# Optimization experiments

Measured on AMD Instinct MI355X. Metric: run time of the kernel, lower is better.

Reference implementation:

```python
import jax, jax.numpy as jnp
import numpy as np

B, T, D = 2, 4096, 512
H = 8
HD = D // H


def setup_inputs() -> dict:
    key = jax.random.key(0)
    ks = jax.random.split(key, 6)
    s = 0.02
    return {
        "token_embed": jax.random.normal(ks[0], (B, T, D), jnp.float32),
        "Wq": jax.random.normal(ks[1], (D, D), jnp.float32) * s,
        "Wk": jax.random.normal(ks[2], (D, D), jnp.float32) * s,
        "Wv": jax.random.normal(ks[3], (D, D), jnp.float32) * s,
        "Wo": jax.random.normal(ks[4], (D, D), jnp.float32) * s,
        "bo": jnp.zeros((D,), jnp.float32),
    }


def reference(token_embed, Wq, Wk, Wv, Wo, bo):
    b, t, d_in = token_embed.shape
    # QKV projections (Linear without bias): x @ W^T with W stored [d_out, d_in]
    q = jnp.einsum("btd,ed->bte", token_embed, Wq).reshape(b, t, H, HD).transpose(0, 2, 1, 3)
    k = jnp.einsum("btd,ed->bte", token_embed, Wk).reshape(b, t, H, HD).transpose(0, 2, 1, 3)
    v = jnp.einsum("btd,ed->bte", token_embed, Wv).reshape(b, t, H, HD).transpose(0, 2, 1, 3)
    # Scores [b, h, t, t] with causal mask applied before scaling (as in source)
    scores = jnp.einsum("bhqd,bhkd->bhqk", q, k)
    causal = jnp.tril(jnp.ones((t, t), bool))  # True = keep
    scores = jnp.where(causal, scores, -jnp.inf)
    attn = jax.nn.softmax(scores / jnp.sqrt(jnp.float32(HD)), axis=-1)
    # dropout p=0.0 -> identity
    ctx = jnp.einsum("bhqk,bhkd->bhqd", attn, v)
    ctx = ctx.transpose(0, 2, 1, 3).reshape(b, t, H * HD)
    return jnp.einsum("btd,ed->bte", ctx, Wo) + bo
```

## Files before the change

### kernel.cpp

```cpp
#include <hip/hip_runtime.h>

#define B_  2
#define T_  4096
#define D_  512
#define H_  8
#define HD_ 64
#define M_  (B_*T_)

typedef _Float16 h16;
typedef _Float16 v8h __attribute__((ext_vector_type(8)));
typedef _Float16 v4h __attribute__((ext_vector_type(4)));
typedef _Float16 h2  __attribute__((ext_vector_type(2)));
typedef float v4f __attribute__((ext_vector_type(4)));
typedef unsigned short us;
typedef unsigned short us8 __attribute__((ext_vector_type(8)));

union PaU { v8h v; h2 p[4]; };

#define AS1 __attribute__((address_space(1)))
#define AS3 __attribute__((address_space(3)))

__device__ __forceinline__ float bf2f(us u){
  union { unsigned int i; float f; } v; v.i = ((unsigned int)u) << 16; return v.f;
}
__device__ __forceinline__ us f2bf(float f){
  union { float f; unsigned int u; } v; v.f = f;
  unsigned int r = v.u + 0x7FFFu + ((v.u >> 16) & 1u);
  return (us)(r >> 16);
}
__device__ __forceinline__ v4f zero4(){ v4f z; z[0]=0.f; z[1]=0.f; z[2]=0.f; z[3]=0.f; return z; }

__device__ __forceinline__ void glds16(const h16* g, h16* l){
  __builtin_amdgcn_global_load_lds((const AS1 int*)(const void*)g,
                                   (AS3 int*)(void*)l, 16, 0, 0);
}

__device__ __forceinline__ h2 pkrtz(float a, float b){
  auto t = __builtin_amdgcn_cvt_pkrtz(a, b);
  h2 r; __builtin_memcpy(&r, &t, sizeof(r)); return r;
}

#define MFMA32 __builtin_amdgcn_mfma_f32_16x16x32_f16

__global__ __launch_bounds__(256) void conv_all(
    const void* __restrict__ x, const void* __restrict__ w0, const void* __restrict__ w1,
    const void* __restrict__ w2, const void* __restrict__ w3, const void* __restrict__ bo,
    h16* __restrict__ xb, h16* __restrict__ d0, h16* __restrict__ d1,
    h16* __restrict__ d2, h16* __restrict__ d3, float* __restrict__ bof)
{
  const int bid = blockIdx.x, tid = threadIdx.x;
  const void* src; int e0; int seg;
  h16* dst = nullptr;
  if (bid < 2048)      { src = x; e0 = bid * 2048; dst = xb; seg = 0; }
  else if (bid < 2560) {
    const int wsel = (bid - 2048) >> 7;
    src = (wsel == 0) ? w0 : (wsel == 1) ? w1 : (wsel == 2) ? w2 : w3;
    dst = (wsel == 0) ? d0 : (wsel == 1) ? d1 : (wsel == 2) ? d2 : d3;
    e0 = ((bid - 2048) & 127) * 2048; seg = 0;
  } else                { src = bo; e0 = 0; seg = 1; }

  __shared__ int sflag;
  if (tid == 0) sflag = 0;
  __syncthreads();
  const float probe = bf2f(((const us*)src)[e0 + tid]);
  if (!(fabsf(probe) < 1e4f)) atomicAdd(&sflag, 1);
  __syncthreads();
  const int isf32 = (sflag != 0);

  if (seg) {
    if (tid < 64) {
      const int i = tid * 8;
#pragma unroll
      for (int e = 0; e < 8; e++)
        bof[i + e] = isf32 ? ((const float*)src)[i + e] : bf2f(((const us*)src)[i + e]);
    }
    return;
  }
  const int i = e0 + tid * 8;
  float v[8];
  if (isf32) {
    const float* pf = (const float*)src + i;
    const float4 a = *(const float4*)pf;
    const float4 c = *(const float4*)(pf + 4);
    v[0]=a.x; v[1]=a.y; v[2]=a.z; v[3]=a.w; v[4]=c.x; v[5]=c.y; v[6]=c.z; v[7]=c.w;
  } else {
    const us8 u = *(const us8*)((const us*)src + i);
#pragma unroll
    for (int e = 0; e < 8; e++) v[e] = bf2f(u[e]);
  }
  v8h o;
#pragma unroll
  for (int e = 0; e < 8; e++) o[e] = (h16)v[e];
  *(v8h*)(dst + i) = o;
}

__device__ __forceinline__ void stage4(const h16* __restrict__ A, const h16* __restrict__ W,
                                       int m0, int n0, int kk, h16* sA, h16* sB, int tid){
  const int colA = (tid & 3) << 3;
  const int rowT = tid >> 2;
#pragma unroll
  for (int rd = 0; rd < 2; rd++) {
    const int row = rd * 64 + rowT;
    const int f = rd * 2048 + tid * 8;
    glds16(A + (size_t)(m0 + row) * D_ + kk + colA, sA + f);
    glds16(W + (size_t)(n0 + row) * D_ + kk + colA, sB + f);
  }
}

__device__ __forceinline__ void gemm_core(const h16* __restrict__ A,
                                          const h16* __restrict__ W,
                                          int m0, int n0, h16* sA, h16* sB,
                                          v4f acc[4][4]) {
  const int tid = threadIdx.x;
  const int lane = tid & 63, wid = tid >> 6;
  const int r = lane & 15, q = lane >> 4;
#pragma unroll
  for (int i = 0; i < 4; i++)
#pragma unroll
    for (int j = 0; j < 4; j++) acc[i][j] = zero4();

  stage4(A, W, m0, n0, 0, sA, sB, tid);
#pragma unroll 1
  for (int kt = 0; kt < 16; kt++) {
    asm volatile("s_waitcnt vmcnt(0)" ::: "memory");
    asm volatile("s_barrier" ::: "memory");
    if (kt < 15) {
      const int nb = (kt + 1) & 1;
      stage4(A, W, m0, n0, (kt + 1) * 32, sA + nb * 4096, sB + nb * 4096, tid);
    }
    const h16* pA = sA + (kt & 1) * 4096 + ((wid & 1) * 64 + r) * 32 + q * 8;
    const h16* pB = sB + (kt & 1) * 4096 + ((wid >> 1) * 64 + r) * 32 + q * 8;
    v8h a[4], b[4];
#pragma unroll
    for (int i = 0; i < 4; i++) a[i] = *(const v8h*)(pA + i * 512);
#pragma unroll
    for (int j = 0; j < 4; j++) b[j] = *(const v8h*)(pB + j * 512);
    __builtin_amdgcn_s_setprio(1);
#pragma unroll
    for (int i = 0; i < 4; i++)
#pragma unroll
      for (int j = 0; j < 4; j++)
        acc[i][j] = MFMA32(a[i], b[j], acc[i][j], 0, 0, 0);
    __builtin_amdgcn_s_setprio(0);
  }
}

__global__ __launch_bounds__(256, 3) void gemm_qkv(
    const h16* __restrict__ X,
    const h16* __restrict__ Wq, const h16* __restrict__ Wk, const h16* __restrict__ Wv,
    h16* __restrict__ Qo, h16* __restrict__ Ko, h16* __restrict__ VTo)
{
  __shared__ h16 sA[2 * 4096], sB[2 * 4096];
  const h16* W = (blockIdx.z == 0) ? Wq : (blockIdx.z == 1 ? Wk : Wv);
  const int m0 = blockIdx.x * 128, n0 = blockIdx.y * 128;
  v4f acc[4][4];
  gemm_core(X, W, m0, n0, sA, sB, acc);
  const int lane = threadIdx.x & 63, wid = threadIdx.x >> 6;
  const int r = lane & 15, q = lane >> 4;
  const int wm = m0 + (wid & 1) * 64, wn = n0 + (wid >> 1) * 64;
  if (blockIdx.z == 2) {
#pragma unroll
    for (int i = 0; i < 4; i++) {
      const int row0 = wm + i * 16 + q * 4;
      const int bb = row0 >> 12, tt0 = row0 & (T_ - 1);
      const int tpermb = (tt0 & ~63) | (q << 3) | ((i & 1) << 2) | ((i >> 1) << 5);
#pragma unroll
      for (int j = 0; j < 4; j++) {
        const int col = wn + j * 16 + r;
        const int hh = col >> 6, hd = col & 63;
        v4h st;
#pragma unroll
        for (int rr = 0; rr < 4; rr++) st[rr] = (h16)acc[i][j][rr];
        *(v4h*)(VTo + ((size_t)(((bb << 3) + hh) << 6) + hd) * T_ + tpermb) = st;
      }
    }
  } else {
    h16* Y = (blockIdx.z == 0) ? Qo : Ko;
    const float sc = (blockIdx.z == 0) ? 0.1803368801f : 1.0f;
#pragma unroll
    for (int i = 0; i < 4; i++)
#pragma unroll
      for (int j = 0; j < 4; j++)
#pragma unroll
        for (int rr = 0; rr < 4; rr++)
          Y[(size_t)(wm + i*16 + q*4 + rr) * D_ + wn + j*16 + r] = (h16)(acc[i][j][rr] * sc);
  }
}

__global__ __launch_bounds__(256, 3) void gemm_out(
    const h16* __restrict__ A, const h16* __restrict__ W,
    const float* __restrict__ bias, void* __restrict__ out, const void* __restrict__ xprobe)
{
  __shared__ h16 sA[2 * 4096], sB[2 * 4096];
  __shared__ int sflag;
  if (threadIdx.x == 0) sflag = 0;
  __syncthreads();
  const float probe = bf2f(((const us*)xprobe)[threadIdx.x]);
  if (!(fabsf(probe) < 1e4f)) atomicAdd(&sflag, 1);
  __syncthreads();
  const int flag = (sflag != 0);

  const int m0 = blockIdx.x * 128, n0 = blockIdx.y * 128;
  v4f acc[4][4];
  gemm_core(A, W, m0, n0, sA, sB, acc);
  const int lane = threadIdx.x & 63, wid = threadIdx.x >> 6;
  const int r = lane & 15, q = lane >> 4;
  const int wm = m0 + (wid & 1) * 64, wn = n0 + (wid >> 1) * 64;
#pragma unroll
  for (int i = 0; i < 4; i++)
#pragma unroll
    for (int j = 0; j < 4; j++)
#pragma unroll
      for (int rr = 0; rr < 4; rr++) {
        const int row = wm + i*16 + q*4 + rr;
        const int col = wn + j*16 + r;
        const float v = acc[i][j][rr] + bias[col];
        if (flag) ((float*)out)[(size_t)row * D_ + col] = v;
        else ((us*)out)[(size_t)row * D_ + col] = f2bf(v);
      }
}

__global__ __launch_bounds__(256, 4) void attn_kernel(
    const h16* __restrict__ Q, const h16* __restrict__ K,
    const h16* __restrict__ VT, h16* __restrict__ Ctx)
{
  const int h = blockIdx.x;
  const int pos = blockIdx.y + (blockIdx.z << 6);
  const int qc = 63 - (pos >> 1);
  const int b  = pos & 1;
  const int tid = threadIdx.x;
  const int wid = tid >> 6, lane = tid & 63;
  const int r = lane & 15, quad = lane >> 4;
  const int kw = wid & 1, qw = wid >> 1;

  const size_t headoff = (size_t)b * T_ * D_ + (size_t)h * HD_;
  const h16* Qh  = Q + headoff;
  const h16* Kh  = K + headoff;
  const h16* VTh = VT + (size_t)(b * H_ + h) * HD_ * T_;
  h16* Ch = Ctx + headoff;

  __shared__ h16 smem[4][4096];

  const int q0 = qc * 64 + qw * 32;
  const int ntiles = qc + 1;

  const v8h aq00 = *(const v8h*)(Qh + (size_t)(q0 + r) * D_ + quad * 8);
  const v8h aq01 = *(const v8h*)(Qh + (size_t)(q0 + r) * D_ + 32 + quad * 8);
  const v8h aq10 = *(const v8h*)(Qh + (size_t)(q0 + 16 + r) * D_ + quad * 8);
  const v8h aq11 = *(const v8h*)(Qh + (size_t)(q0 + 16 + r) * D_ + 32 + quad * 8);

  v8h vone;
#pragma unroll
  for (int e = 0; e < 8; e++) vone[e] = (h16)1;

  v4f o0[4], o1[4];
#pragma unroll
  for (int j = 0; j < 4; j++) { o0[j] = zero4(); o1[j] = zero4(); }
  v4f ld0 = zero4(), ld1 = zero4();

  const int srow = tid >> 3;
  const int sj = (tid & 7) ^ (srow & 7);
  const h16* kcur = Kh + (size_t)srow * D_ + sj * 8;
  const h16* vcur = VTh + (size_t)srow * T_ + sj * 8;

  glds16(kcur, &smem[0][tid * 8]); glds16(kcur + 32 * D_, &smem[0][2048 + tid * 8]);
  glds16(vcur, &smem[2][tid * 8]); glds16(vcur + 32 * T_, &smem[2][2048 + tid * 8]);
  kcur += 64 * D_; vcur += 64;

  const int xo0 = (quad ^ (r & 7)) * 8;
  const int xo1 = ((quad + 4) ^ (r & 7)) * 8;
  const int xov = ((quad + kw * 4) ^ (r & 7)) * 8;
  const int krow = kw * 32 + r;
  const int kloc = kw * 32 + quad * 4;
  const int qlim0 = qw * 32 + r, qlim1 = qw * 32 + 16 + r;

#define ATT_TILE(CB, MASKED) do {                                              \
    const h16* sKc = smem[(CB)];                                               \
    const h16* sVc = smem[2 + (CB)];                                           \
    const h16* bK = sKc + krow * 64;                                           \
    const v8h ka0 = *(const v8h*)(bK + xo0);                                   \
    const v8h ka1 = *(const v8h*)(bK + xo1);                                   \
    const v8h ka2 = *(const v8h*)(bK + 16 * 64 + xo0);                         \
    const v8h ka3 = *(const v8h*)(bK + 16 * 64 + xo1);                         \
    v8h va[4];                                                                 \
    _Pragma("unroll")                                                          \
    for (int j = 0; j < 4; j++)                                                \
      va[j] = *(const v8h*)(sVc + (j * 16 + r) * 64 + xov);                    \
    v4f s00 = zero4(), s10 = zero4(), s01 = zero4(), s11 = zero4();            \
    __builtin_amdgcn_s_setprio(1);                                             \
    s00 = MFMA32(ka0, aq00, s00, 0,0,0); s00 = MFMA32(ka1, aq01, s00, 0,0,0);  \
    s10 = MFMA32(ka2, aq00, s10, 0,0,0); s10 = MFMA32(ka3, aq01, s10, 0,0,0);  \
    s01 = MFMA32(ka0, aq10, s01, 0,0,0); s01 = MFMA32(ka1, aq11, s01, 0,0,0);  \
    s11 = MFMA32(ka2, aq10, s11, 0,0,0); s11 = MFMA32(ka3, aq11, s11, 0,0,0);  \
    __builtin_amdgcn_s_setprio(0);                                             \
    PaU pa0, pa1;                                                              \
    _Pragma("unroll")                                                          \
    for (int qb = 0; qb < 2; qb++) {                                           \
      const v4f& sa = qb ? s01 : s00;                                          \
      const v4f& sb = qb ? s11 : s10;                                          \
      const int qlim = qb ? qlim1 : qlim0;                                     \
      float e0[4], e1[4];                                                      \
      _Pragma("unroll")                                                        \
      for (int rr = 0; rr < 4; rr++) {                                         \
        float v0 = sa[rr], v1 = sb[rr];                                        \
        if (MASKED) {                                                          \
          if (kloc + rr > qlim)      v0 = -1e30f;                              \
          if (kloc + 16 + rr > qlim) v1 = -1e30f;                              \
        }                                                                      \
        e0[rr] = exp2f(v0); e1[rr] = exp2f(v1);                                \
      }                                                                        \
      PaU* pa = qb ? &pa1 : &pa0;                                              \
      pa->p[0] = pkrtz(e0[0], e0[1]); pa->p[1] = pkrtz(e0[2], e0[3]);          \
      pa->p[2] = pkrtz(e1[0], e1[1]); pa->p[3] = pkrtz(e1[2], e1[3]);          \
    }                                                                          \
    __builtin_amdgcn_s_setprio(1);                                             \
    ld0 = MFMA32(pa0.v, vone, ld0, 0,0,0);                                     \
    ld1 = MFMA32(pa1.v, vone, ld1, 0,0,0);                                     \
    _Pragma("unroll")                                                          \
    for (int j = 0; j < 4; j++) {                                              \
      o0[j] = MFMA32(pa0.v, va[j], o0[j], 0,0,0);                              \
      o1[j] = MFMA32(pa1.v, va[j], o1[j], 0,0,0);                              \
    }                                                                          \
    __builtin_amdgcn_s_setprio(0);                                             \
  } while(0)

#pragma unroll 1
  for (int kt = 0; kt < ntiles - 1; kt++) {
    asm volatile("s_waitcnt vmcnt(0)" ::: "memory");
    asm volatile("s_barrier" ::: "memory");
    const int nb = (kt + 1) & 1;
    glds16(kcur, &smem[nb][tid * 8]);
    glds16(kcur + 32 * D_, &smem[nb][2048 + tid * 8]);
    glds16(vcur, &smem[2 + nb][tid * 8]);
    glds16(vcur + 32 * T_, &smem[2 + nb][2048 + tid * 8]);
    kcur += 64 * D_; vcur += 64;
    ATT_TILE(kt & 1, false);
  }
  asm volatile("s_waitcnt vmcnt(0)" ::: "memory");
  asm volatile("s_barrier" ::: "memory");
  ATT_TILE((ntiles - 1) & 1, true);
#undef ATT_TILE

  __syncthreads();
  float* const red = (float*)&smem[0][0];
  float* const seg = red + qw * 2112;
  float* const lred = red + 4224;
  if (kw) {
#pragma unroll
    for (int hdb = 0; hdb < 4; hdb++)
#pragma unroll
      for (int j = 0; j < 4; j++) {
        seg[(quad * 4 + j) * 66 + hdb * 16 + r] = o0[hdb][j];
        seg[(16 + quad * 4 + j) * 66 + hdb * 16 + r] = o1[hdb][j];
      }
    if (r == 0) {
#pragma unroll
      for (int j = 0; j < 4; j++) {
        lred[qw * 32 + quad * 4 + j] = ld0[j];
        lred[qw * 32 + 16 + quad * 4 + j] = ld1[j];
      }
    }
  }
  __syncthreads();
  if (!kw) {
    float inv0[4], inv1[4];
#pragma unroll
    for (int j = 0; j < 4; j++) {
      inv0[j] = 1.0f / (ld0[j] + lred[qw * 32 + quad * 4 + j]);
      inv1[j] = 1.0f / (ld1[j] + lred[qw * 32 + 16 + quad * 4 + j]);
    }
#pragma unroll
    for (int hdb = 0; hdb < 4; hdb++)
#pragma unroll
      for (int j = 0; j < 4; j++) {
        const float a0 = o0[hdb][j] + seg[(quad * 4 + j) * 66 + hdb * 16 + r];
        const float a1 = o1[hdb][j] + seg[(16 + quad * 4 + j) * 66 + hdb * 16 + r];
        Ch[(size_t)(q0 + quad * 4 + j) * D_ + hdb * 16 + r] = (h16)(a0 * inv0[j]);
        Ch[(size_t)(q0 + 16 + quad * 4 + j) * D_ + hdb * 16 + r] = (h16)(a1 * inv1[j]);
      }
  }
}

extern "C" void kernel_launch(void* const* d_in, const int* in_sizes, int n_in,
                              void* d_out, int out_size, void* d_ws, size_t ws_size,
                              hipStream_t stream) {
  char* ws = (char*)d_ws;
  h16* xb  = (h16*)(ws + 0);
  h16* qb  = (h16*)(ws + 8388608);
  h16* kb  = (h16*)(ws + 16777216);
  h16* vt  = (h16*)(ws + 25165824);
  h16* ctx = (h16*)(ws + 33554432);
  h16* wqb = (h16*)(ws + 41943040);
  h16* wkb = (h16*)(ws + 41943040 + 524288);
  h16* wvb = (h16*)(ws + 41943040 + 2 * 524288);
  h16* wob = (h16*)(ws + 41943040 + 3 * 524288);
  float* bof = (float*)(ws + 41943040 + 4 * 524288);

  conv_all<<<2561, 256, 0, stream>>>(d_in[0], d_in[1], d_in[2], d_in[3], d_in[4],
                                     d_in[5], xb, wqb, wkb, wvb, wob, bof);
  gemm_qkv<<<dim3(M_ / 128, D_ / 128, 3), 256, 0, stream>>>(xb, wqb, wkb, wvb, qb, kb, vt);
  attn_kernel<<<dim3(H_, 64, B_), 256, 0, stream>>>(qb, kb, vt, ctx);
  gemm_out<<<dim3(M_ / 128, D_ / 128, 1), 256, 0, stream>>>(ctx, wob, bof, d_out, d_in[0]);
}
```

Baseline: 172.7 us.

## Shrink GEMM M-tile to 64 and overlap next-tile loads with compute

Both projection GEMMs move from 128x128 to 64x128 block tiles, doubling the grid and raising the occupancy target from 3 to 4 blocks per CU. The staging loop now issues the next k-slice prefetch before waiting, uses a partial vmcnt wait so global loads overlap the MFMA work, and adds a trailing barrier to guard the double buffer. The aim is better CU fill and latency hiding for these small GEMMs, at the cost of lower per-block reuse of the weight tile and an extra barrier per iteration.

```diff
diff --git a/kernel.cpp b/kernel.cpp
--- a/kernel.cpp
+++ b/kernel.cpp
@@ -94,76 +94,76 @@
   *(v8h*)(dst + i) = o;
 }
 
-__device__ __forceinline__ void stage4(const h16* __restrict__ A, const h16* __restrict__ W,
+__device__ __forceinline__ void stage3(const h16* __restrict__ A, const h16* __restrict__ W,
                                        int m0, int n0, int kk, h16* sA, h16* sB, int tid){
-  const int colA = (tid & 3) << 3;
-  const int rowT = tid >> 2;
-#pragma unroll
-  for (int rd = 0; rd < 2; rd++) {
-    const int row = rd * 64 + rowT;
-    const int f = rd * 2048 + tid * 8;
-    glds16(A + (size_t)(m0 + row) * D_ + kk + colA, sA + f);
-    glds16(W + (size_t)(n0 + row) * D_ + kk + colA, sB + f);
-  }
-}
-
-__device__ __forceinline__ void gemm_core(const h16* __restrict__ A,
-                                          const h16* __restrict__ W,
-                                          int m0, int n0, h16* sA, h16* sB,
-                                          v4f acc[4][4]) {
+  const int col = (tid & 3) << 3;
+  const int row = tid >> 2;
+  glds16(A + (size_t)(m0 + row) * D_ + kk + col, sA + tid * 8);
+  glds16(W + (size_t)(n0 + row) * D_ + kk + col, sB + tid * 8);
+  glds16(W + (size_t)(n0 + 64 + row) * D_ + kk + col, sB + 2048 + tid * 8);
+}
+
+__device__ __forceinline__ void gemm_core64(const h16* __restrict__ A,
+                                            const h16* __restrict__ W,
+                                            int m0, int n0, h16* sA, h16* sB,
+                                            v4f acc[2][4]) {
   const int tid = threadIdx.x;
   const int lane = tid & 63, wid = tid >> 6;
   const int r = lane & 15, q = lane >> 4;
 #pragma unroll
-  for (int i = 0; i < 4; i++)
+  for (int i = 0; i < 2; i++)
 #pragma unroll
     for (int j = 0; j < 4; j++) acc[i][j] = zero4();
 
-  stage4(A, W, m0, n0, 0, sA, sB, tid);
+  stage3(A, W, m0, n0, 0, sA, sB, tid);
 #pragma unroll 1
   for (int kt = 0; kt < 16; kt++) {
-    asm volatile("s_waitcnt vmcnt(0)" ::: "memory");
-    asm volatile("s_barrier" ::: "memory");
     if (kt < 15) {
       const int nb = (kt + 1) & 1;
-      stage4(A, W, m0, n0, (kt + 1) * 32, sA + nb * 4096, sB + nb * 4096, tid);
+      stage3(A, W, m0, n0, (kt + 1) * 32, sA + nb * 2048, sB + nb * 4096, tid);
+      asm volatile("s_waitcnt vmcnt(3)" ::: "memory");
+    } else {
+      asm volatile("s_waitcnt vmcnt(0)" ::: "memory");
     }
-    const h16* pA = sA + (kt & 1) * 4096 + ((wid & 1) * 64 + r) * 32 + q * 8;
+    asm volatile("s_barrier" ::: "memory");
+    const h16* pA = sA + (kt & 1) * 2048 + ((wid & 1) * 32 + r) * 32 + q * 8;
     const h16* pB = sB + (kt & 1) * 4096 + ((wid >> 1) * 64 + r) * 32 + q * 8;
-    v8h a[4], b[4];
-#pragma unroll
-    for (int i = 0; i < 4; i++) a[i] = *(const v8h*)(pA + i * 512);
+    v8h a[2], b[4];
+#pragma unroll
+    for (int i = 0; i < 2; i++) a[i] = *(const v8h*)(pA + i * 512);
 #pragma unroll
     for (int j = 0; j < 4; j++) b[j] = *(const v8h*)(pB + j * 512);
     __builtin_amdgcn_s_setprio(1);
 #pragma unroll
-    for (int i = 0; i < 4; i++)
+    for (int i = 0; i < 2; i++)
 #pragma unroll
       for (int j = 0; j < 4; j++)
         acc[i][j] = MFMA32(a[i], b[j], acc[i][j], 0, 0, 0);
     __builtin_amdgcn_s_setprio(0);
-  }
-}
-
-__global__ __launch_bounds__(256, 3) void gemm_qkv(
+    asm volatile("s_barrier" ::: "memory");
+  }
+}
+
+__global__ __launch_bounds__(256, 4) void gemm_qkv(
     const h16* __restrict__ X,
     const h16* __restrict__ Wq, const h16* __restrict__ Wk, const h16* __restrict__ Wv,
     h16* __restrict__ Qo, h16* __restrict__ Ko, h16* __restrict__ VTo)
 {
-  __shared__ h16 sA[2 * 4096], sB[2 * 4096];
+  __shared__ h16 sA[2 * 2048], sB[2 * 4096];
   const h16* W = (blockIdx.z == 0) ? Wq : (blockIdx.z == 1 ? Wk : Wv);
-  const int m0 = blockIdx.x * 128, n0 = blockIdx.y * 128;
-  v4f acc[4][4];
-  gemm_core(X, W, m0, n0, sA, sB, acc);
+  const int m0 = blockIdx.x * 64, n0 = blockIdx.y * 128;
+  v4f acc[2][4];
+  gemm_core64(X, W, m0, n0, sA, sB, acc);
   const int lane = threadIdx.x & 63, wid = threadIdx.x >> 6;
   const int r = lane & 15, q = lane >> 4;
-  const int wm = m0 + (wid & 1) * 64, wn = n0 + (wid >> 1) * 64;
+  const int wm = m0 + (wid & 1) * 32, wn = n0 + (wid >> 1) * 64;
   if (blockIdx.z == 2) {
 #pragma unroll
-    for (int i = 0; i < 4; i++) {
+    for (int i = 0; i < 2; i++) {
+      const int iold = (wid & 1) * 2 + i;
       const int row0 = wm + i * 16 + q * 4;
       const int bb = row0 >> 12, tt0 = row0 & (T_ - 1);
-      const int tpermb = (tt0 & ~63) | (q << 3) | ((i & 1) << 2) | ((i >> 1) << 5);
+      const int tpermb = (tt0 & ~63) | (q << 3) | ((iold & 1) << 2) | ((iold >> 1) << 5);
 #pragma unroll
       for (int j = 0; j < 4; j++) {
         const int col = wn + j * 16 + r;
@@ -178,7 +178,7 @@
     h16* Y = (blockIdx.z == 0) ? Qo : Ko;
     const float sc = (blockIdx.z == 0) ? 0.1803368801f : 1.0f;
 #pragma unroll
-    for (int i = 0; i < 4; i++)
+    for (int i = 0; i < 2; i++)
 #pragma unroll
       for (int j = 0; j < 4; j++)
 #pragma unroll
@@ -187,11 +187,11 @@
   }
 }
 
-__global__ __launch_bounds__(256, 3) void gemm_out(
+__global__ __launch_bounds__(256, 4) void gemm_out(
     const h16* __restrict__ A, const h16* __restrict__ W,
     const float* __restrict__ bias, void* __restrict__ out, const void* __restrict__ xprobe)
 {
-  __shared__ h16 sA[2 * 4096], sB[2 * 4096];
+  __shared__ h16 sA[2 * 2048], sB[2 * 4096];
   __shared__ int sflag;
   if (threadIdx.x == 0) sflag = 0;
   __syncthreads();
@@ -200,14 +200,14 @@
   __syncthreads();
   const int flag = (sflag != 0);
 
-  const int m0 = blockIdx.x * 128, n0 = blockIdx.y * 128;
-  v4f acc[4][4];
-  gemm_core(A, W, m0, n0, sA, sB, acc);
+  const int m0 = blockIdx.x * 64, n0 = blockIdx.y * 128;
+  v4f acc[2][4];
+  gemm_core64(A, W, m0, n0, sA, sB, acc);
   const int lane = threadIdx.x & 63, wid = threadIdx.x >> 6;
   const int r = lane & 15, q = lane >> 4;
-  const int wm = m0 + (wid & 1) * 64, wn = n0 + (wid >> 1) * 64;
-#pragma unroll
-  for (int i = 0; i < 4; i++)
+  const int wm = m0 + (wid & 1) * 32, wn = n0 + (wid >> 1) * 64;
+#pragma unroll
+  for (int i = 0; i < 2; i++)
 #pragma unroll
     for (int j = 0; j < 4; j++)
 #pragma unroll
@@ -398,7 +398,7 @@
 
   conv_all<<<2561, 256, 0, stream>>>(d_in[0], d_in[1], d_in[2], d_in[3], d_in[4],
                                      d_in[5], xb, wqb, wkb, wvb, wob, bof);
-  gemm_qkv<<<dim3(M_ / 128, D_ / 128, 3), 256, 0, stream>>>(xb, wqb, wkb, wvb, qb, kb, vt);
+  gemm_qkv<<<dim3(M_ / 64, D_ / 128, 3), 256, 0, stream>>>(xb, wqb, wkb, wvb, qb, kb, vt);
   attn_kernel<<<dim3(H_, 64, B_), 256, 0, stream>>>(qb, kb, vt, ctx);
-  gemm_out<<<dim3(M_ / 128, D_ / 128, 1), 256, 0, stream>>>(ctx, wob, bof, d_out, d_in[0]);
-}
+  gemm_out<<<dim3(M_ / 64, D_ / 128, 1), 256, 0, stream>>>(ctx, wob, bof, d_out, d_in[0]);
+}
```

New measurement: 172.7 us. No clear change (+0.0%).

## Overlap GEMM prefetch with compute, swap grid order, split V transpose into kernel

Applied to the files above, without the earlier changes.

The GEMM main loop now issues the next tile's global loads before waiting, and waits only on the older loads (vmcnt(4)). A second barrier after the MFMAs protects buffer reuse. The grid is reordered so adjacent blocks share the same A rows, which is meant to improve L2 reuse. The V projection now stores row-major into the ctx buffer, and a separate vt_transpose kernel writes the permuted transposed layout through LDS. This replaces the scattered strided stores in the GEMM epilogue, at the cost of an extra launch and an extra pass over V.

```diff
diff --git a/kernel.cpp b/kernel.cpp
--- a/kernel.cpp
+++ b/kernel.cpp
@@ -122,12 +122,14 @@
   stage4(A, W, m0, n0, 0, sA, sB, tid);
 #pragma unroll 1
   for (int kt = 0; kt < 16; kt++) {
-    asm volatile("s_waitcnt vmcnt(0)" ::: "memory");
-    asm volatile("s_barrier" ::: "memory");
     if (kt < 15) {
       const int nb = (kt + 1) & 1;
       stage4(A, W, m0, n0, (kt + 1) * 32, sA + nb * 4096, sB + nb * 4096, tid);
+      asm volatile("s_waitcnt vmcnt(4)" ::: "memory");
+    } else {
+      asm volatile("s_waitcnt vmcnt(0)" ::: "memory");
     }
+    asm volatile("s_barrier" ::: "memory");
     const h16* pA = sA + (kt & 1) * 4096 + ((wid & 1) * 64 + r) * 32 + q * 8;
     const h16* pB = sB + (kt & 1) * 4096 + ((wid >> 1) * 64 + r) * 32 + q * 8;
     v8h a[4], b[4];
@@ -135,55 +137,67 @@
     for (int i = 0; i < 4; i++) a[i] = *(const v8h*)(pA + i * 512);
 #pragma unroll
     for (int j = 0; j < 4; j++) b[j] = *(const v8h*)(pB + j * 512);
-    __builtin_amdgcn_s_setprio(1);
 #pragma unroll
     for (int i = 0; i < 4; i++)
 #pragma unroll
       for (int j = 0; j < 4; j++)
         acc[i][j] = MFMA32(a[i], b[j], acc[i][j], 0, 0, 0);
-    __builtin_amdgcn_s_setprio(0);
+    asm volatile("s_barrier" ::: "memory");
   }
 }
 
 __global__ __launch_bounds__(256, 3) void gemm_qkv(
     const h16* __restrict__ X,
     const h16* __restrict__ Wq, const h16* __restrict__ Wk, const h16* __restrict__ Wv,
-    h16* __restrict__ Qo, h16* __restrict__ Ko, h16* __restrict__ VTo)
+    h16* __restrict__ Qo, h16* __restrict__ Ko, h16* __restrict__ Vo)
 {
   __shared__ h16 sA[2 * 4096], sB[2 * 4096];
   const h16* W = (blockIdx.z == 0) ? Wq : (blockIdx.z == 1 ? Wk : Wv);
-  const int m0 = blockIdx.x * 128, n0 = blockIdx.y * 128;
+  const int n0 = blockIdx.x * 128, m0 = blockIdx.y * 128;
   v4f acc[4][4];
   gemm_core(X, W, m0, n0, sA, sB, acc);
   const int lane = threadIdx.x & 63, wid = threadIdx.x >> 6;
   const int r = lane & 15, q = lane >> 4;
   const int wm = m0 + (wid & 1) * 64, wn = n0 + (wid >> 1) * 64;
-  if (blockIdx.z == 2) {
-#pragma unroll
-    for (int i = 0; i < 4; i++) {
-      const int row0 = wm + i * 16 + q * 4;
-      const int bb = row0 >> 12, tt0 = row0 & (T_ - 1);
-      const int tpermb = (tt0 & ~63) | (q << 3) | ((i & 1) << 2) | ((i >> 1) << 5);
-#pragma unroll
-      for (int j = 0; j < 4; j++) {
-        const int col = wn + j * 16 + r;
-        const int hh = col >> 6, hd = col & 63;
-        v4h st;
-#pragma unroll
-        for (int rr = 0; rr < 4; rr++) st[rr] = (h16)acc[i][j][rr];
-        *(v4h*)(VTo + ((size_t)(((bb << 3) + hh) << 6) + hd) * T_ + tpermb) = st;
-      }
+  h16* Y = (blockIdx.z == 0) ? Qo : (blockIdx.z == 1 ? Ko : Vo);
+  const float sc = (blockIdx.z == 0) ? 0.1803368801f : 1.0f;
+#pragma unroll
+  for (int i = 0; i < 4; i++)
+#pragma unroll
+    for (int j = 0; j < 4; j++)
+#pragma unroll
+      for (int rr = 0; rr < 4; rr++)
+        Y[(size_t)(wm + i*16 + q*4 + rr) * D_ + wn + j*16 + r] = (h16)(acc[i][j][rr] * sc);
+}
+
+__global__ __launch_bounds__(256) void vt_transpose(
+    const h16* __restrict__ V, h16* __restrict__ VT)
+{
+  __shared__ h16 tile[64 * 66];
+  const int bh = blockIdx.y;
+  const int t0 = blockIdx.x * 64;
+  const int u = threadIdx.x;
+  const int b = bh >> 3, h = bh & 7;
+  const h16* src = V + ((size_t)(b * T_ + t0)) * D_ + h * 64;
+#pragma unroll
+  for (int rep = 0; rep < 2; rep++) {
+    const int w = rep * 256 + u;
+    const int row = w >> 3, ch = w & 7;
+    *(v8h*)(tile + row * 66 + ch * 8) = *(const v8h*)(src + (size_t)row * D_ + ch * 8);
+  }
+  __syncthreads();
+  h16* dst = VT + ((size_t)bh * 64) * T_ + t0;
+#pragma unroll
+  for (int rep = 0; rep < 2; rep++) {
+    const int w = rep * 256 + u;
+    const int hd = w >> 3, c = w & 7;
+    v8h st;
+#pragma unroll
+    for (int e = 0; e < 8; e++) {
+      const int t6 = (e & 3) + (c & 3) * 4 + (e >> 2) * 16 + (c >> 2) * 32;
+      st[e] = tile[t6 * 66 + hd];
     }
-  } else {
-    h16* Y = (blockIdx.z == 0) ? Qo : Ko;
-    const float sc = (blockIdx.z == 0) ? 0.1803368801f : 1.0f;
-#pragma unroll
-    for (int i = 0; i < 4; i++)
-#pragma unroll
-      for (int j = 0; j < 4; j++)
-#pragma unroll
-        for (int rr = 0; rr < 4; rr++)
-          Y[(size_t)(wm + i*16 + q*4 + rr) * D_ + wn + j*16 + r] = (h16)(acc[i][j][rr] * sc);
+    *(v8h*)(dst + (size_t)hd * T_ + c * 8) = st;
   }
 }
 
@@ -200,7 +214,7 @@
   __syncthreads();
   const int flag = (sflag != 0);
 
-  const int m0 = blockIdx.x * 128, n0 = blockIdx.y * 128;
+  const int n0 = blockIdx.x * 128, m0 = blockIdx.y * 128;
   v4f acc[4][4];
   gemm_core(A, W, m0, n0, sA, sB, acc);
   const int lane = threadIdx.x & 63, wid = threadIdx.x >> 6;
@@ -398,7 +412,8 @@
 
   conv_all<<<2561, 256, 0, stream>>>(d_in[0], d_in[1], d_in[2], d_in[3], d_in[4],
                                      d_in[5], xb, wqb, wkb, wvb, wob, bof);
-  gemm_qkv<<<dim3(M_ / 128, D_ / 128, 3), 256, 0, stream>>>(xb, wqb, wkb, wvb, qb, kb, vt);
+  gemm_qkv<<<dim3(D_ / 128, M_ / 128, 3), 256, 0, stream>>>(xb, wqb, wkb, wvb, qb, kb, ctx);
+  vt_transpose<<<dim3(T_ / 64, B_ * H_), 256, 0, stream>>>(ctx, vt);
   attn_kernel<<<dim3(H_, 64, B_), 256, 0, stream>>>(qb, kb, vt, ctx);
-  gemm_out<<<dim3(M_ / 128, D_ / 128, 1), 256, 0, stream>>>(ctx, wob, bof, d_out, d_in[0]);
-}
+  gemm_out<<<dim3(D_ / 128, M_ / 128, 1), 256, 0, stream>>>(ctx, wob, bof, d_out, d_in[0]);
+}
```

Result: slower. 176.6 us (+2.3%).
